# Kernel optimization log

Hardware: AMD Instinct MI355X
Metric: run time of the kernel (lower is better)

The kernel has to match this reference:

```python
import jax, jax.numpy as jnp
import numpy as np

B, NORM_NC, LABEL_NC, H, W, SL = 8, 256, 19, 64, 64, 512
EPS = 1e-5


def _conv5(x, w, b):
    # 5x5 'same' conv, NCHW / OIHW
    y = jax.lax.conv_general_dilated(x, w, (1, 1), [(2, 2), (2, 2)],
                                     dimension_numbers=('NCHW', 'OIHW', 'NCHW'))
    return y + b[None, :, None, None]


def _instance_norm(x):
    # InstanceNorm2d(affine=False): per-sample, per-channel over HxW, biased var
    m = x.mean(axis=(2, 3), keepdims=True)
    v = x.var(axis=(2, 3), keepdims=True)
    return (x - m) / jnp.sqrt(v + EPS)


def setup_inputs() -> dict:
    key = jax.random.key(0)
    ks = jax.random.split(key, 12)
    # one-hot semantic segmentation map (what segmap.bool() assumes in practice)
    labels = jax.random.randint(ks[0], (B, H, W), 0, LABEL_NC)
    segmap = jax.nn.one_hot(labels, LABEL_NC, axis=1, dtype=jnp.float32)  # [B,19,H,W]
    s = 0.02
    return {
        'x': jax.random.normal(ks[1], (B, NORM_NC, H, W), jnp.float32),
        'segmap': segmap,
        'style_codes': jax.random.normal(ks[2], (B, LABEL_NC, SL), jnp.float32),
        'fc_w': jax.random.normal(ks[3], (LABEL_NC, SL, SL), jnp.float32) * s,
        'fc_b': jnp.zeros((LABEL_NC, SL), jnp.float32),
        'conv_gamma_w': jax.random.normal(ks[4], (NORM_NC, SL, 5, 5), jnp.float32) * s,
        'conv_gamma_b': jnp.zeros((NORM_NC,), jnp.float32),
        'conv_beta_w': jax.random.normal(ks[5], (NORM_NC, SL, 5, 5), jnp.float32) * s,
        'conv_beta_b': jnp.zeros((NORM_NC,), jnp.float32),
        'spade_shared_w': jax.random.normal(ks[6], (512, LABEL_NC, 5, 5), jnp.float32) * s,
        'spade_shared_b': jnp.zeros((512,), jnp.float32),
        'spade_gamma_w': jax.random.normal(ks[7], (NORM_NC, 512, 5, 5), jnp.float32) * s,
        'spade_gamma_b': jnp.zeros((NORM_NC,), jnp.float32),
        'spade_beta_w': jax.random.normal(ks[8], (NORM_NC, 512, 5, 5), jnp.float32) * s,
        'spade_beta_b': jnp.zeros((NORM_NC,), jnp.float32),
        'blending_gamma': jnp.zeros((1,), jnp.float32),
        'blending_beta': jnp.zeros((1,), jnp.float32),
    }


def reference(x, segmap, style_codes, fc_w, fc_b,
              conv_gamma_w, conv_gamma_b, conv_beta_w, conv_beta_b,
              spade_shared_w, spade_shared_b,
              spade_gamma_w, spade_gamma_b, spade_beta_w, spade_beta_b,
              blending_gamma, blending_beta):
    normalized = _instance_norm(x)
    # F.interpolate(segmap, size=x.shape[2:], mode='nearest') is identity here
    # (segmap already has x's spatial size).
    mask = segmap > 0  # segmap.bool(): [B,J,H,W]
    J = mask.shape[1]

    # per-class style MLP: mu[b,j] = relu(fc_mu_j(style_codes[b,j]))
    mu = jax.nn.relu(jnp.einsum('bjd,jed->bje', style_codes, fc_w) + fc_b)  # [B,J,SL]

    # for overlapping masks; pixels with no class stay zero.
    last_idx = (J - 1) - jnp.argmax(mask[:, ::-1], axis=1)  # [B,H,W] last true j
    any_m = mask.any(axis=1)                                 # [B,H,W]
    mu_sel = mu[jnp.arange(mu.shape[0])[:, None, None], last_idx]  # [B,H,W,SL]
    middle_avg = jnp.where(any_m[..., None], mu_sel, 0.0).transpose(0, 3, 1, 2)

    gamma_avg = _conv5(middle_avg, conv_gamma_w, conv_gamma_b)
    beta_avg = _conv5(middle_avg, conv_beta_w, conv_beta_b)

    actv = jax.nn.relu(_conv5(segmap, spade_shared_w, spade_shared_b))
    gamma_spade = _conv5(actv, spade_gamma_w, spade_gamma_b)
    beta_spade = _conv5(actv, spade_beta_w, spade_beta_b)

    ga = jax.nn.sigmoid(blending_gamma)  # shape (1,) broadcasts
    ba = jax.nn.sigmoid(blending_beta)
    gamma_final = ga * gamma_avg + (1 - ga) * gamma_spade
    beta_final = ba * beta_avg + (1 - ba) * beta_spade
    return normalized * (1 + gamma_final) + beta_final
```

## Files before the change

### kernel.cpp

```cpp
#include <hip/hip_runtime.h>
#include <hip/hip_bf16.h>
#include <stdint.h>

typedef __attribute__((__ext_vector_type__(8))) __bf16 bf16x8;
typedef __attribute__((__ext_vector_type__(2))) __bf16 bf16x2;
typedef __attribute__((__ext_vector_type__(4))) float  f32x4;
typedef __attribute__((__ext_vector_type__(8))) int    v8i;

#define SCALE_A_DW 0x77777777
#define SCALE_B_DW 0x79797979

__device__ __forceinline__ void gl_lds16(const void* g, void* l) {
  __builtin_amdgcn_global_load_lds(
      (__attribute__((address_space(1))) void*)(uintptr_t)g,
      (__attribute__((address_space(3))) void*)(unsigned)(uintptr_t)l,
      16, 0, 0);
}

__global__ __launch_bounds__(256) void k_prep(
    const float* __restrict__ x, float* __restrict__ stats,
    const float* __restrict__ seg, int* __restrict__ labels,
    const float* __restrict__ cgw, const float* __restrict__ cbw,
    float* __restrict__ wpa,
    const float* __restrict__ ssw, __bf16* __restrict__ wspb,
    __bf16* __restrict__ Aav) {
  __shared__ __align__(16) char smem[16*401*4];
  int blk = blockIdx.x;
  if (blk < 2048) {
    int bc = blk;
    const float4* p = (const float4*)(x + (size_t)bc * 4096);
    float s = 0.f, ss = 0.f;
    for (int i = threadIdx.x; i < 1024; i += 256) {
      float4 v = p[i];
      s  += v.x + v.y + v.z + v.w;
      ss += v.x*v.x + v.y*v.y + v.z*v.z + v.w*v.w;
    }
    #pragma unroll
    for (int o = 32; o > 0; o >>= 1) { s += __shfl_down(s, o); ss += __shfl_down(ss, o); }
    float* sh = (float*)smem;
    int wv = threadIdx.x >> 6;
    if ((threadIdx.x & 63) == 0) { sh[wv] = s; sh[4 + wv] = ss; }
    __syncthreads();
    if (threadIdx.x == 0) {
      float S = sh[0]+sh[1]+sh[2]+sh[3], SS = sh[4]+sh[5]+sh[6]+sh[7];
      float m = S * (1.f/4096.f);
      float var = SS * (1.f/4096.f) - m*m;
      stats[bc] = m;
      stats[2048 + bc] = rsqrtf(var + 1e-5f);
    }
  } else if (blk < 2176) {
    int idx = (blk - 2048)*256 + threadIdx.x;
    int b = idx >> 12, pix = idx & 4095;
    const float* p = seg + (size_t)b*19*4096 + pix;
    int lab = -1;
    for (int j = 0; j < 19; ++j) if (p[(size_t)j*4096] > 0.f) lab = j;
    labels[idx] = lab;
  } else if (blk < 3200) {
    int bid = blk - 2176;
    float* s = (float*)smem;
    int n0 = (bid & 31) * 16, c0 = (bid >> 5) * 16;
    for (int i = threadIdx.x; i < 6400; i += 256) {
      int nn = i / 400, qq = i % 400;
      int n = n0 + nn;
      const float* src = (n < 256) ? cgw + (size_t)n*12800 : cbw + (size_t)(n-256)*12800;
      s[nn*401 + qq] = src[c0*25 + qq];
    }
    __syncthreads();
    for (int i = threadIdx.x; i < 6400; i += 256) {
      int nn = i & 15, rest = i >> 4;
      int k5 = rest % 25, cc = rest / 25;
      wpa[((size_t)k5*512 + c0 + cc)*512 + n0 + nn] = s[nn*401 + cc*25 + k5];
    }
  } else if (blk < 4200) {
    int idx = (blk - 3200)*256 + threadIdx.x;
    int o = idx & 511, k5 = (idx >> 9) % 25, j = idx / 12800;
    wspb[idx] = (j < 19) ? (__bf16)ssw[((size_t)o*19 + j)*25 + k5] : (__bf16)0.f;
  } else {
    ((unsigned*)(Aav + 3800ull*512))[threadIdx.x] = 0;
  }
}

__global__ __launch_bounds__(512) void k_mu(const float* __restrict__ sc,
                                            const float* __restrict__ fcw,
                                            const float* __restrict__ fcb,
                                            float* __restrict__ mu) {
  int b = blockIdx.x / 19, j = blockIdx.x % 19;
  __shared__ float s[512];
  s[threadIdx.x] = sc[(b*19 + j)*512 + threadIdx.x];
  __syncthreads();
  int e = threadIdx.x;
  const float4* w4 = (const float4*)(fcw + ((size_t)(j*512 + e))*512);
  const float4* s4 = (const float4*)s;
  float acc = 0.f;
  for (int d = 0; d < 128; ++d) {
    float4 w = w4[d], v = s4[d];
    acc += w.x*v.x + w.y*v.y + w.z*v.z + w.w*v.w;
  }
  acc += fcb[j*512 + e];
  mu[(b*19 + j)*512 + e] = fmaxf(acc, 0.f);
}

__global__ __launch_bounds__(256) void k_pack_spade(
    const float* __restrict__ g, const float* __restrict__ bt,
    uint8_t* __restrict__ wq) {
  int n = blockIdx.x;
  const float* src = (n < 256) ? g + (size_t)n*12800 : bt + (size_t)(n-256)*12800;
  __shared__ float s[12800];
  for (int i = threadIdx.x; i < 12800; i += 256) s[i] = src[i];
  __syncthreads();
  int t = threadIdx.x;
  for (int k5 = 0; k5 < 25; ++k5) {
    float w0 = s[(2*t)*25 + k5] * 64.f, w1 = s[(2*t+1)*25 + k5] * 64.f;
    int pk = __builtin_amdgcn_cvt_pk_fp8_f32(w0, w1, 0, false);
    *(unsigned short*)(wq + ((size_t)k5*512 + n)*512 + 2*t) = (unsigned short)pk;
  }
}

__global__ __launch_bounds__(512) void k_A_avg(const float* __restrict__ mu,
                                               const float* __restrict__ wpa,
                                               __bf16* __restrict__ A) {
  int b = blockIdx.x / 25, k5 = blockIdx.x % 25;
  int n = threadIdx.x;
  const float* wp = wpa + (size_t)k5*262144 + n;
  const float* mub = mu + b*19*512;
  float acc[19];
  #pragma unroll
  for (int j = 0; j < 19; ++j) acc[j] = 0.f;
  for (int c = 0; c < 512; ++c) {
    float w = wp[(size_t)c*512];
    #pragma unroll
    for (int j = 0; j < 19; ++j) acc[j] += mub[j*512 + c] * w;
  }
  #pragma unroll
  for (int j = 0; j < 19; ++j)
    A[((size_t)((b*19 + j)*25 + k5))*512 + n] = (__bf16)acc[j];
}

__global__ void k_actv(const int* __restrict__ labels, const __bf16* __restrict__ wsp,
                       const float* __restrict__ ssb, uint8_t* __restrict__ actv) {
  int b = blockIdx.x / 68, hp = blockIdx.x % 68;
  int t = threadIdx.x;
  size_t rowbase = ((size_t)b*68 + hp)*68;
  if (hp < 2 || hp >= 66) {
    unsigned* dp = (unsigned*)(actv + rowbase*512);
    for (int i = t; i < 8704; i += 256) dp[i] = 0;
    return;
  }
  int h = hp - 2;
  __shared__ int lab[5*68];
  for (int i = t; i < 5*68; i += 256) {
    int dh = i / 68, xx = i % 68;
    int hh = h + dh - 2, ww = xx - 2;
    int l = 19;
    if (hh >= 0 && hh < 64 && ww >= 0 && ww < 64) {
      int l0 = labels[b*4096 + hh*64 + ww];
      if (l0 >= 0) l = l0;
    }
    lab[i] = l;
  }
  {
    unsigned* dp = (unsigned*)(actv + rowbase*512);
    dp[t] = 0; dp[66*128 + t] = 0;
  }
  __syncthreads();
  float bs0 = ssb[2*t], bs1 = ssb[2*t + 1];
  for (int w = 0; w < 64; ++w) {
    float a0 = bs0, a1 = bs1;
    #pragma unroll
    for (int tap = 0; tap < 25; ++tap) {
      int l = lab[(tap/5)*68 + w + (tap%5)];
      bf16x2 v = *(const bf16x2*)(wsp + (size_t)(l*25 + tap)*512 + 2*t);
      a0 += (float)v[0]; a1 += (float)v[1];
    }
    a0 = fmaxf(a0, 0.f) * 256.f;
    a1 = fmaxf(a1, 0.f) * 256.f;
    int pk = __builtin_amdgcn_cvt_pk_fp8_f32(a0, a1, 0, false);
    *(unsigned short*)(actv + (rowbase + 2 + w)*512 + 2*t) = (unsigned short)pk;
  }
}

__global__ __launch_bounds__(256) void k_conv(
    const uint8_t* __restrict__ actv, const uint8_t* __restrict__ wq,
    const float* __restrict__ sgb, const float* __restrict__ sbb,
    __bf16* __restrict__ gbs) {
  __shared__ __align__(16) uint8_t ldsA[2][16384];
  __shared__ __align__(16) uint8_t ldsB[2][16384];
  const int tid = threadIdx.x, wv = tid >> 6, lane = tid & 63;
  const int l15 = lane & 15, q = lane >> 4;
  const int m0 = blockIdx.x * 128, n0 = blockIdx.y * 128;
  const int b = m0 >> 12;

  int aoff[4], boff[4];
  #pragma unroll
  for (int i = 0; i < 4; ++i) {
    int p = (wv*4 + i)*64 + lane;
    int r = p >> 3, pc = p & 7;
    int cl = pc ^ (r & 7);
    int pix = (m0 + r) & 4095;
    int h = pix >> 6, w = pix & 63;
    aoff[i] = ((b*68 + h)*68 + w)*512 + cl*16;
    boff[i] = (n0 + r)*512 + cl*16;
  }

  const int wm = (wv >> 1) * 64, wn = (wv & 1) * 64;
  f32x4 acc[4][4] = {};

  auto stage = [&](int t, int buf) {
    int k5 = t >> 2, kc = t & 3;
    int a_k = ((k5/5)*68 + (k5%5))*512 + kc*128;
    int b_k = k5*262144 + kc*128;
    uint8_t* la = &ldsA[buf][0];
    uint8_t* lb = &ldsB[buf][0];
    #pragma unroll
    for (int i = 0; i < 4; ++i) {
      gl_lds16(actv + aoff[i] + a_k, la + (wv*4 + i)*1024);
      gl_lds16(wq   + boff[i] + b_k, lb + (wv*4 + i)*1024);
    }
  };

  auto compute = [&](int buf) {
    v8i bfr[4];
    #pragma unroll
    for (int ni = 0; ni < 4; ++ni) {
      int row = wn + ni*16 + l15;
      const uint8_t* base = &ldsB[buf][row*128];
      union { v8i v; uint4 u[2]; } tt;
      tt.u[0] = *(const uint4*)(base + ((2*q    ) ^ (row & 7))*16);
      tt.u[1] = *(const uint4*)(base + ((2*q + 1) ^ (row & 7))*16);
      bfr[ni] = tt.v;
    }
    #pragma unroll
    for (int mi = 0; mi < 4; ++mi) {
      int row = wm + mi*16 + l15;
      const uint8_t* base = &ldsA[buf][row*128];
      union { v8i v; uint4 u[2]; } tt;
      tt.u[0] = *(const uint4*)(base + ((2*q    ) ^ (row & 7))*16);
      tt.u[1] = *(const uint4*)(base + ((2*q + 1) ^ (row & 7))*16);
      v8i af = tt.v;
      #pragma unroll
      for (int ni = 0; ni < 4; ++ni)
        acc[mi][ni] = __builtin_amdgcn_mfma_scale_f32_16x16x128_f8f6f4(
            af, bfr[ni], acc[mi][ni], 0, 0, 0, SCALE_A_DW, 0, SCALE_B_DW);
    }
  };

  stage(0, 0);
  __syncthreads();
  for (int tt = 0; tt < 50; ++tt) {
    int t = 2*tt;
    stage(t + 1, 1);
    compute(0);
    __syncthreads();
    if (tt < 49) stage(t + 2, 0);
    compute(1);
    __syncthreads();
  }

  #pragma unroll
  for (int ni = 0; ni < 4; ++ni) {
    int n = n0 + wn + ni*16 + l15;
    float bias = (n < 256) ? sgb[n] : sbb[n - 256];
    #pragma unroll
    for (int mi = 0; mi < 4; ++mi) {
      int m = m0 + wm + mi*16 + q*4;
      size_t base = (size_t)m*512 + n;
      #pragma unroll
      for (int r = 0; r < 4; ++r)
        gbs[base + (size_t)r*512] = (__bf16)(acc[mi][ni][r] + bias);
    }
  }
}

__global__ void k_gather(const int* __restrict__ labels, const __bf16* __restrict__ A,
                         const float* __restrict__ cgb, const float* __restrict__ cbb,
                         __bf16* __restrict__ gba) {
  int wt = blockIdx.x & 3, h = (blockIdx.x >> 2) & 63, b = blockIdx.x >> 8;
  int w0 = wt * 16;
  __shared__ int rowbase[5*20];
  for (int i = threadIdx.x; i < 100; i += 256) {
    int dh = i / 20, xx = i % 20;
    int hh = h + dh - 2, ww = w0 + xx - 2;
    int l = (hh >= 0 && hh < 64 && ww >= 0 && ww < 64) ? labels[b*4096 + hh*64 + ww] : -1;
    rowbase[i] = (l >= 0) ? (b*19 + l)*25 : -1;
  }
  __syncthreads();
  int t = threadIdx.x;
  float bs0, bs1;
  if (2*t < 256) { bs0 = cgb[2*t]; bs1 = cgb[2*t + 1]; }
  else           { bs0 = cbb[2*t - 256]; bs1 = cbb[2*t - 255]; }
  for (int px = 0; px < 16; ++px) {
    float a0 = bs0, a1 = bs1;
    #pragma unroll
    for (int tap = 0; tap < 25; ++tap) {
      int rb = rowbase[(tap/5)*20 + px + (tap%5)];
      int row = (rb >= 0) ? rb + tap : 3800;
      bf16x2 v = *(const bf16x2*)(A + (size_t)row*512 + 2*t);
      a0 += (float)v[0]; a1 += (float)v[1];
    }
    size_t o = ((size_t)b*4096 + h*64 + w0 + px) * 512;
    bf16x2 r; r[0] = (__bf16)a0; r[1] = (__bf16)a1;
    *(bf16x2*)(gba + o + 2*t) = r;
  }
}

__global__ __launch_bounds__(256) void k_final(
    const float* __restrict__ x, const float* __restrict__ stats,
    const __bf16* __restrict__ gba, const __bf16* __restrict__ gbs,
    const float* __restrict__ blg, const float* __restrict__ blb,
    float* __restrict__ out) {
  __shared__ __bf16 tg_av[64*66], tb_av[64*66], tg_sp[64*66], tb_sp[64*66];
  int bidx = blockIdx.x;
  int pt = bidx & 63, ct = (bidx >> 6) & 3, b = bidx >> 8;
  int c0 = ct*64, p0 = pt*64;
  for (int i = threadIdx.x; i < 4096; i += 256) {
    int p = i >> 6, c = i & 63;
    size_t src = ((size_t)b*4096 + p0 + p)*512;
    int d = p*66 + c;
    tg_av[d] = gba[src + c0 + c];
    tb_av[d] = gba[src + 256 + c0 + c];
    tg_sp[d] = gbs[src + c0 + c];
    tb_sp[d] = gbs[src + 256 + c0 + c];
  }
  __syncthreads();
  float ga = 1.f / (1.f + expf(-blg[0]));
  float ba = 1.f / (1.f + expf(-blb[0]));
  int p = threadIdx.x & 63;
  for (int cl = threadIdx.x >> 6; cl < 64; cl += 4) {
    int c = c0 + cl;
    int bc = b*256 + c;
    float mean = stats[bc], rstd = stats[2048 + bc];
    size_t o = (size_t)bc*4096 + p0 + p;
    int d = p*66 + cl;
    float gf  = ga*(float)tg_av[d] + (1.f - ga)*(float)tg_sp[d];
    float bf_ = ba*(float)tb_av[d] + (1.f - ba)*(float)tb_sp[d];
    out[o] = (x[o] - mean)*rstd*(1.f + gf) + bf_;
  }
}

extern "C" void kernel_launch(void* const* d_in, const int* in_sizes, int n_in,
                              void* d_out, int out_size, void* d_ws, size_t ws_size,
                              hipStream_t stream) {
  const float* x    = (const float*)d_in[0];
  const float* seg  = (const float*)d_in[1];
  const float* sc   = (const float*)d_in[2];
  const float* fcw  = (const float*)d_in[3];
  const float* fcb  = (const float*)d_in[4];
  const float* cgw  = (const float*)d_in[5];
  const float* cgb  = (const float*)d_in[6];
  const float* cbw  = (const float*)d_in[7];
  const float* cbb  = (const float*)d_in[8];
  const float* ssw  = (const float*)d_in[9];
  const float* ssb  = (const float*)d_in[10];
  const float* sgw  = (const float*)d_in[11];
  const float* sgb  = (const float*)d_in[12];
  const float* sbw  = (const float*)d_in[13];
  const float* sbb  = (const float*)d_in[14];
  const float* blg  = (const float*)d_in[15];
  const float* blb  = (const float*)d_in[16];
  float* out = (float*)d_out;

  char* ws = (char*)d_ws;
  size_t off = 0;
  auto alloc = [&](size_t bytes) {
    void* p = ws + off; off += (bytes + 255) & ~(size_t)255; return p;
  };
  float*   stats = (float*)alloc(2048ull*2*4);
  int*     labels= (int*)  alloc(32768ull*4);
  float*   mu    = (float*)alloc(77824ull*4);
  __bf16*  Aav   = (__bf16*)alloc((3800ull + 1)*512*2);
  __bf16*  wspb  = (__bf16*)alloc(20ull*25*512*2);
  float*   wpa   = (float*)alloc(25ull*512*512*4);
  uint8_t* wq    = (uint8_t*)alloc(25ull*512*512);
  uint8_t* actv  = (uint8_t*)alloc(8ull*68*68*512);
  __bf16*  gba   = (__bf16*)alloc(8ull*4096*512*2);
  __bf16*  gbs   = (__bf16*)alloc(8ull*4096*512*2);

  k_prep      <<<4201, 256, 0, stream>>>(x, stats, seg, labels, cgw, cbw, wpa, ssw, wspb, Aav);
  k_mu        <<<152, 512, 0, stream>>>(sc, fcw, fcb, mu);
  k_pack_spade<<<512, 256, 0, stream>>>(sgw, sbw, wq);
  k_A_avg     <<<200, 512, 0, stream>>>(mu, wpa, Aav);
  k_actv      <<<544, 256, 0, stream>>>(labels, wspb, ssb, actv);
  k_conv      <<<dim3(256, 4), 256, 0, stream>>>(actv, wq, sgb, sbb, gbs);
  k_gather    <<<2048, 256, 0, stream>>>(labels, Aav, cgb, cbb, gba);
  k_final     <<<2048, 256, 0, stream>>>(x, stats, gba, gbs, blg, blb, out);
}
```

Baseline: 667.7 us.

## Enlarge FP8 conv tiles with pipelined waits and fuse gather into final epilogue

The FP8 MFMA conv now uses 256x256 tiles with 512 threads and 8x4 accumulators per wave. It keeps two LDS buffers in flight using explicit vmcnt waits, raw barriers and setprio around the MFMA block. The gather of the averaged-style conv is fused with the final blend and normalization kernel, which drops the gba intermediate and one full-size write and read. Risks include the 128KB LDS footprint and higher register pressure lowering occupancy, and the conv grid shrinking to 256 blocks.

```diff
diff --git a/kernel.cpp b/kernel.cpp
--- a/kernel.cpp
+++ b/kernel.cpp
@@ -179,31 +179,32 @@
   }
 }
 
-__global__ __launch_bounds__(256) void k_conv(
+__global__ __launch_bounds__(512) void k_conv(
     const uint8_t* __restrict__ actv, const uint8_t* __restrict__ wq,
     const float* __restrict__ sgb, const float* __restrict__ sbb,
     __bf16* __restrict__ gbs) {
-  __shared__ __align__(16) uint8_t ldsA[2][16384];
-  __shared__ __align__(16) uint8_t ldsB[2][16384];
+  __shared__ __align__(16) uint8_t ldsA[2][32768];
+  __shared__ __align__(16) uint8_t ldsB[2][32768];
   const int tid = threadIdx.x, wv = tid >> 6, lane = tid & 63;
   const int l15 = lane & 15, q = lane >> 4;
-  const int m0 = blockIdx.x * 128, n0 = blockIdx.y * 128;
+  const int m0 = blockIdx.x * 256, n0 = blockIdx.y * 256;
   const int b = m0 >> 12;
 
-  int aoff[4], boff[4];
+  int aoff[4], boff[4], ldst[4];
   #pragma unroll
   for (int i = 0; i < 4; ++i) {
-    int p = (wv*4 + i)*64 + lane;
+    int p = i*512 + tid;
     int r = p >> 3, pc = p & 7;
     int cl = pc ^ (r & 7);
     int pix = (m0 + r) & 4095;
     int h = pix >> 6, w = pix & 63;
     aoff[i] = ((b*68 + h)*68 + w)*512 + cl*16;
     boff[i] = (n0 + r)*512 + cl*16;
-  }
-
-  const int wm = (wv >> 1) * 64, wn = (wv & 1) * 64;
-  f32x4 acc[4][4] = {};
+    ldst[i] = i*8192 + wv*1024;
+  }
+
+  const int wm = (wv >> 2) * 128, wn = (wv & 3) * 64;
+  f32x4 acc[8][4] = {};
 
   auto stage = [&](int t, int buf) {
     int k5 = t >> 2, kc = t & 3;
@@ -213,8 +214,8 @@
     uint8_t* lb = &ldsB[buf][0];
     #pragma unroll
     for (int i = 0; i < 4; ++i) {
-      gl_lds16(actv + aoff[i] + a_k, la + (wv*4 + i)*1024);
-      gl_lds16(wq   + boff[i] + b_k, lb + (wv*4 + i)*1024);
+      gl_lds16(actv + aoff[i] + a_k, la + ldst[i]);
+      gl_lds16(wq   + boff[i] + b_k, lb + ldst[i]);
     }
   };
 
@@ -229,8 +230,9 @@
       tt.u[1] = *(const uint4*)(base + ((2*q + 1) ^ (row & 7))*16);
       bfr[ni] = tt.v;
     }
-    #pragma unroll
-    for (int mi = 0; mi < 4; ++mi) {
+    __builtin_amdgcn_s_setprio(1);
+    #pragma unroll
+    for (int mi = 0; mi < 8; ++mi) {
       int row = wm + mi*16 + l15;
       const uint8_t* base = &ldsA[buf][row*128];
       union { v8i v; uint4 u[2]; } tt;
@@ -242,26 +244,45 @@
         acc[mi][ni] = __builtin_amdgcn_mfma_scale_f32_16x16x128_f8f6f4(
             af, bfr[ni], acc[mi][ni], 0, 0, 0, SCALE_A_DW, 0, SCALE_B_DW);
     }
+    __builtin_amdgcn_s_setprio(0);
   };
 
   stage(0, 0);
-  __syncthreads();
-  for (int tt = 0; tt < 50; ++tt) {
-    int t = 2*tt;
-    stage(t + 1, 1);
+  stage(1, 1);
+  #pragma unroll 1
+  for (int t = 0; t < 98; t += 2) {
+    asm volatile("s_waitcnt vmcnt(8)" ::: "memory");
+    __builtin_amdgcn_s_barrier();
+    __builtin_amdgcn_sched_barrier(0);
     compute(0);
-    __syncthreads();
-    if (tt < 49) stage(t + 2, 0);
+    __builtin_amdgcn_sched_barrier(0);
+    __builtin_amdgcn_s_barrier();
+    __builtin_amdgcn_sched_barrier(0);
+    stage(t + 2, 0);
+    asm volatile("s_waitcnt vmcnt(8)" ::: "memory");
+    __builtin_amdgcn_s_barrier();
+    __builtin_amdgcn_sched_barrier(0);
     compute(1);
-    __syncthreads();
-  }
+    __builtin_amdgcn_sched_barrier(0);
+    __builtin_amdgcn_s_barrier();
+    __builtin_amdgcn_sched_barrier(0);
+    stage(t + 3, 1);
+  }
+  asm volatile("s_waitcnt vmcnt(8)" ::: "memory");
+  __builtin_amdgcn_s_barrier();
+  __builtin_amdgcn_sched_barrier(0);
+  compute(0);
+  asm volatile("s_waitcnt vmcnt(0)" ::: "memory");
+  __builtin_amdgcn_s_barrier();
+  __builtin_amdgcn_sched_barrier(0);
+  compute(1);
 
   #pragma unroll
   for (int ni = 0; ni < 4; ++ni) {
     int n = n0 + wn + ni*16 + l15;
     float bias = (n < 256) ? sgb[n] : sbb[n - 256];
     #pragma unroll
-    for (int mi = 0; mi < 4; ++mi) {
+    for (int mi = 0; mi < 8; ++mi) {
       int m = m0 + wm + mi*16 + q*4;
       size_t base = (size_t)m*512 + n;
       #pragma unroll
@@ -271,12 +292,17 @@
   }
 }
 
-__global__ void k_gather(const int* __restrict__ labels, const __bf16* __restrict__ A,
-                         const float* __restrict__ cgb, const float* __restrict__ cbb,
-                         __bf16* __restrict__ gba) {
+__global__ __launch_bounds__(256) void k_gf(
+    const int* __restrict__ labels, const __bf16* __restrict__ A,
+    const float* __restrict__ cgb, const float* __restrict__ cbb,
+    const __bf16* __restrict__ gbs, const float* __restrict__ x,
+    const float* __restrict__ stats, const float* __restrict__ blg,
+    const float* __restrict__ blb, float* __restrict__ out) {
   int wt = blockIdx.x & 3, h = (blockIdx.x >> 2) & 63, b = blockIdx.x >> 8;
   int w0 = wt * 16;
   __shared__ int rowbase[5*20];
+  __shared__ __bf16 avg[16][512];
+  __shared__ __bf16 spd[16][512];
   for (int i = threadIdx.x; i < 100; i += 256) {
     int dh = i / 20, xx = i % 20;
     int hh = h + dh - 2, ww = w0 + xx - 2;
@@ -288,6 +314,7 @@
   float bs0, bs1;
   if (2*t < 256) { bs0 = cgb[2*t]; bs1 = cgb[2*t + 1]; }
   else           { bs0 = cbb[2*t - 256]; bs1 = cbb[2*t - 255]; }
+  size_t pixb = (size_t)b*4096 + h*64 + w0;
   for (int px = 0; px < 16; ++px) {
     float a0 = bs0, a1 = bs1;
     #pragma unroll
@@ -297,43 +324,30 @@
       bf16x2 v = *(const bf16x2*)(A + (size_t)row*512 + 2*t);
       a0 += (float)v[0]; a1 += (float)v[1];
     }
-    size_t o = ((size_t)b*4096 + h*64 + w0 + px) * 512;
-    bf16x2 r; r[0] = (__bf16)a0; r[1] = (__bf16)a1;
-    *(bf16x2*)(gba + o + 2*t) = r;
-  }
-}
-
-__global__ __launch_bounds__(256) void k_final(
-    const float* __restrict__ x, const float* __restrict__ stats,
-    const __bf16* __restrict__ gba, const __bf16* __restrict__ gbs,
-    const float* __restrict__ blg, const float* __restrict__ blb,
-    float* __restrict__ out) {
-  __shared__ __bf16 tg_av[64*66], tb_av[64*66], tg_sp[64*66], tb_sp[64*66];
-  int bidx = blockIdx.x;
-  int pt = bidx & 63, ct = (bidx >> 6) & 3, b = bidx >> 8;
-  int c0 = ct*64, p0 = pt*64;
-  for (int i = threadIdx.x; i < 4096; i += 256) {
-    int p = i >> 6, c = i & 63;
-    size_t src = ((size_t)b*4096 + p0 + p)*512;
-    int d = p*66 + c;
-    tg_av[d] = gba[src + c0 + c];
-    tb_av[d] = gba[src + 256 + c0 + c];
-    tg_sp[d] = gbs[src + c0 + c];
-    tb_sp[d] = gbs[src + 256 + c0 + c];
+    avg[px][2*t]     = (__bf16)a0;
+    avg[px][2*t + 1] = (__bf16)a1;
+    *(bf16x2*)&spd[px][2*t] = *(const bf16x2*)(gbs + (pixb + px)*512 + 2*t);
   }
   __syncthreads();
   float ga = 1.f / (1.f + expf(-blg[0]));
   float ba = 1.f / (1.f + expf(-blb[0]));
-  int p = threadIdx.x & 63;
-  for (int cl = threadIdx.x >> 6; cl < 64; cl += 4) {
-    int c = c0 + cl;
-    int bc = b*256 + c;
-    float mean = stats[bc], rstd = stats[2048 + bc];
-    size_t o = (size_t)bc*4096 + p0 + p;
-    int d = p*66 + cl;
-    float gf  = ga*(float)tg_av[d] + (1.f - ga)*(float)tg_sp[d];
-    float bf_ = ba*(float)tb_av[d] + (1.f - ba)*(float)tb_sp[d];
-    out[o] = (x[o] - mean)*rstd*(1.f + gf) + bf_;
+  int c = threadIdx.x;
+  int bc = b*256 + c;
+  float mean = stats[bc], rstd = stats[2048 + bc];
+  size_t xb = (size_t)bc*4096 + h*64 + w0;
+  #pragma unroll
+  for (int pq = 0; pq < 4; ++pq) {
+    float4 xv = *(const float4*)(x + xb + pq*4);
+    float4 ov;
+    float* xo = (float*)&xv; float* oo = (float*)&ov;
+    #pragma unroll
+    for (int j = 0; j < 4; ++j) {
+      int px = pq*4 + j;
+      float gf  = ga*(float)avg[px][c]       + (1.f - ga)*(float)spd[px][c];
+      float bf_ = ba*(float)avg[px][256 + c] + (1.f - ba)*(float)spd[px][256 + c];
+      oo[j] = (xo[j] - mean)*rstd*(1.f + gf) + bf_;
+    }
+    *(float4*)(out + xb + pq*4) = ov;
   }
 }
 
@@ -372,7 +386,6 @@
   float*   wpa   = (float*)alloc(25ull*512*512*4);
   uint8_t* wq    = (uint8_t*)alloc(25ull*512*512);
   uint8_t* actv  = (uint8_t*)alloc(8ull*68*68*512);
-  __bf16*  gba   = (__bf16*)alloc(8ull*4096*512*2);
   __bf16*  gbs   = (__bf16*)alloc(8ull*4096*512*2);
 
   k_prep      <<<4201, 256, 0, stream>>>(x, stats, seg, labels, cgw, cbw, wpa, ssw, wspb, Aav);
@@ -380,7 +393,6 @@
   k_pack_spade<<<512, 256, 0, stream>>>(sgw, sbw, wq);
   k_A_avg     <<<200, 512, 0, stream>>>(mu, wpa, Aav);
   k_actv      <<<544, 256, 0, stream>>>(labels, wspb, ssb, actv);
-  k_conv      <<<dim3(256, 4), 256, 0, stream>>>(actv, wq, sgb, sbb, gbs);
-  k_gather    <<<2048, 256, 0, stream>>>(labels, Aav, cgb, cbb, gba);
-  k_final     <<<2048, 256, 0, stream>>>(x, stats, gba, gbs, blg, blb, out);
-}
+  k_conv      <<<dim3(128, 2), 512, 0, stream>>>(actv, wq, sgb, sbb, gbs);
+  k_gf        <<<2048, 256, 0, stream>>>(labels, Aav, cgb, cbb, gbs, x, stats, blg, blb, out);
+}
```

Result: faster. 641.4 us (-3.9%).
